# Performance work log

Hardware: AMD Instinct MI355X
Metric: run time of the kernel (lower is better)

## Reference

```python
import jax, jax.numpy as jnp
import numpy as np

T, D, H, E, K = 8192, 1024, 4096, 8, 2


def setup_inputs() -> dict:
    key = jax.random.key(0)
    ks = jax.random.split(key, 6)
    s_in = 1.0 / np.sqrt(D)
    s_hid = 1.0 / np.sqrt(H)
    return {
        "hidden_states": jax.random.normal(ks[0], (T, D), dtype=jnp.float32),
        "router_w": jax.random.normal(ks[1], (D, E), dtype=jnp.float32) * s_in,
        "expert_w1": jax.random.normal(ks[2], (E, D, H), dtype=jnp.float32) * s_in,
        "expert_w2": jax.random.normal(ks[3], (E, H, D), dtype=jnp.float32) * s_hid,
        "shared_w1": jax.random.normal(ks[4], (D, H), dtype=jnp.float32) * s_in,
        "shared_w2": jax.random.normal(ks[5], (H, D), dtype=jnp.float32) * s_hid,
    }


def reference(hidden_states, router_w, expert_w1, expert_w2, shared_w1, shared_w2):
    x = hidden_states  # [T, D]
    # --- router: softmax over experts, keep top-k, renormalize ---
    probs = jax.nn.softmax(x @ router_w, axis=-1)            # [T, E]
    top_v, top_i = jax.lax.top_k(probs, K)                   # [T, K]
    top_v = top_v / jnp.sum(top_v, axis=-1, keepdims=True)
    # dense combine weights [T, E]; zero for non-selected experts
    comb = jnp.zeros((x.shape[0], E), x.dtype).at[
        jnp.arange(x.shape[0])[:, None], top_i].set(top_v)
    # --- routed experts (dense reference for grouped GEMM) ---
    h = jax.nn.silu(jnp.einsum('td,edh->eth', x, expert_w1))  # [E, T, H]
    eo = jnp.einsum('eth,ehd->etd', h, expert_w2)             # [E, T, D]
    routed = jnp.einsum('te,etd->td', comb, eo)               # [T, D]
    # --- shared expert, always active ---
    shared = jax.nn.silu(x @ shared_w1) @ shared_w2           # [T, D]
    return routed + shared
```

## Files before the change

### kernel.cpp

```cpp
#include <hip/hip_runtime.h>
#include <hip/hip_bf16.h>
#include <stdint.h>

typedef unsigned short u16;
typedef __attribute__((ext_vector_type(8))) short bf16x8;
typedef __attribute__((ext_vector_type(4))) float f32x4;

constexpr int T_ = 8192;
constexpr int D_ = 1024;
constexpr int H_ = 4096;
constexpr int E_ = 8;
constexpr int NT_M  = 104;
constexpr int MAXR  = NT_M * 256;

__device__ __forceinline__ unsigned int f2bf_bits(float f) {
  unsigned int u = __float_as_uint(f);
  return (u + 0x7fffu + ((u >> 16) & 1u)) >> 16;
}
__device__ __forceinline__ float bf2f(u16 b) {
  return __uint_as_float(((unsigned int)b) << 16);
}

__device__ __forceinline__ void load_lds16(const void* g, void* s) {
  __builtin_amdgcn_global_load_lds(
      (const __attribute__((address_space(1))) unsigned int*)g,
      (__attribute__((address_space(3))) unsigned int*)s, 16, 0, 0);
}

__global__ __launch_bounds__(256) void router_kernel(
    const float* __restrict__ x, const float* __restrict__ rw,
    int* __restrict__ counts, int* __restrict__ tok2, float* __restrict__ wgt2) {
  __shared__ float rw_s[E_ * D_];
  __shared__ int c_s[E_];
  const int tid = threadIdx.x;
  if (tid < E_) c_s[tid] = 0;
  for (int f = tid; f < 2048; f += 256) {
    int d = f >> 1, p = f & 1;
    float4 v = *(const float4*)(rw + d * 8 + p * 4);
    rw_s[(p * 4 + 0) * D_ + d] = v.x;
    rw_s[(p * 4 + 1) * D_ + d] = v.y;
    rw_s[(p * 4 + 2) * D_ + d] = v.z;
    rw_s[(p * 4 + 3) * D_ + d] = v.w;
  }
  __syncthreads();
  const int wid = tid >> 6, lane = tid & 63;
  for (int ti = 0; ti < 16; ++ti) {
    const int t = blockIdx.x * 64 + wid * 16 + ti;
    const float* xr = x + (long)t * D_;
    float acc[E_] = {0.f, 0.f, 0.f, 0.f, 0.f, 0.f, 0.f, 0.f};
    for (int j = 0; j < 16; ++j) {
      const int d = lane + 64 * j;
      const float xv = xr[d];
#pragma unroll
      for (int e = 0; e < E_; ++e) acc[e] += xv * rw_s[e * D_ + d];
    }
#pragma unroll
    for (int off = 32; off >= 1; off >>= 1) {
#pragma unroll
      for (int e = 0; e < E_; ++e) acc[e] += __shfl_xor(acc[e], off, 64);
    }
    if (lane == 0) {
      int i0 = 0; float l0 = acc[0];
#pragma unroll
      for (int e = 1; e < E_; ++e) if (acc[e] > l0) { l0 = acc[e]; i0 = e; }
      int i1 = -1; float l1 = -3.4e38f;
#pragma unroll
      for (int e = 0; e < E_; ++e) if (e != i0 && acc[e] > l1) { l1 = acc[e]; i1 = e; }
      const float r = __expf(l1 - l0);
      const float inv = 1.f / (1.f + r);
      tok2[2 * t] = i0; tok2[2 * t + 1] = i1;
      wgt2[2 * t] = inv; wgt2[2 * t + 1] = r * inv;
      atomicAdd(&c_s[i0], 1); atomicAdd(&c_s[i1], 1);
    }
  }
  __syncthreads();
  if (tid < E_) atomicAdd(&counts[tid], c_s[tid]);
}

__global__ void scan_kernel(const int* __restrict__ counts, int* __restrict__ offs,
                            int* __restrict__ tile_expert, int* __restrict__ rowtok) {
  __shared__ int so[10];
  const int tid = threadIdx.x;
  if (tid == 0) {
    int o = 0;
    for (int e = 0; e < E_; ++e) { so[e] = o; o += ((counts[e] + 255) >> 8) << 8; }
    so[8] = o;
    o += T_;
    so[9] = o;
    for (int i = 0; i < 10; ++i) offs[i] = so[i];
  }
  __syncthreads();
  for (int i = tid; i < NT_M; i += 256) {
    const int row = i << 8;
    int e;
    if (row < so[8]) {
      e = 7;
      for (int k = 0; k < 7; ++k) if (row < so[k + 1]) { e = k; break; }
    } else if (row < so[9]) {
      e = 8;
    } else {
      e = -1;
    }
    tile_expert[i] = e;
  }
  for (int r = tid; r < MAXR; r += 256) rowtok[r] = 0;
}

__global__ __launch_bounds__(256) void assign_kernel(
    const int* __restrict__ tok2, const int* __restrict__ offs,
    int* __restrict__ cursors, int* __restrict__ rowtok, int* __restrict__ pos2) {
  __shared__ int lcnt[E_], lbase[E_];
  const int tid = threadIdx.x;
  if (tid < E_) lcnt[tid] = 0;
  __syncthreads();
  const int t = blockIdx.x * 256 + tid;
  const int e0 = tok2[2 * t], e1 = tok2[2 * t + 1];
  const int s0 = atomicAdd(&lcnt[e0], 1);
  const int s1 = atomicAdd(&lcnt[e1], 1);
  __syncthreads();
  if (tid < E_) lbase[tid] = offs[tid] + atomicAdd(&cursors[tid], lcnt[tid]);
  __syncthreads();
  const int p0 = lbase[e0] + s0, p1 = lbase[e1] + s1;
  rowtok[p0] = t; rowtok[p1] = t;
  pos2[2 * t] = p0; pos2[2 * t + 1] = p1;
  rowtok[offs[8] + t] = t;
}

__global__ __launch_bounds__(256) void cvt_x_kernel(const float* __restrict__ x,
                                                    u16* __restrict__ xb) {
  const long i = ((long)blockIdx.x * 256 + threadIdx.x) * 4;
  const float4 v = *(const float4*)(x + i);
  ushort4 o;
  o.x = (u16)f2bf_bits(v.x); o.y = (u16)f2bf_bits(v.y);
  o.z = (u16)f2bf_bits(v.z); o.w = (u16)f2bf_bits(v.w);
  *(ushort4*)(xb + i) = o;
}

__global__ __launch_bounds__(256) void transpose_cvt_kernel(
    const float* __restrict__ src8, const float* __restrict__ srcShared,
    u16* __restrict__ dst, int R, int C) {
  __shared__ float tile[64][65];
  const long stride = (long)R * C;
  const float* src = (blockIdx.z < 8) ? src8 + (long)blockIdx.z * stride : srcShared;
  u16* d = dst + (long)blockIdx.z * stride;
  const int tid = threadIdx.x;
  const int r0 = blockIdx.y * 64, c0 = blockIdx.x * 64;
  const int lr = tid >> 4, lc4 = tid & 15;
#pragma unroll
  for (int p = 0; p < 4; ++p) {
    const float4 v = *(const float4*)(src + (long)(r0 + lr + 16 * p) * C + c0 + lc4 * 4);
    tile[lr + 16 * p][lc4 * 4 + 0] = v.x;
    tile[lr + 16 * p][lc4 * 4 + 1] = v.y;
    tile[lr + 16 * p][lc4 * 4 + 2] = v.z;
    tile[lr + 16 * p][lc4 * 4 + 3] = v.w;
  }
  __syncthreads();
#pragma unroll
  for (int p = 0; p < 4; ++p) {
    const int rr = lr + 16 * p;
    ushort4 o;
    o.x = (u16)f2bf_bits(tile[lc4 * 4 + 0][rr]);
    o.y = (u16)f2bf_bits(tile[lc4 * 4 + 1][rr]);
    o.z = (u16)f2bf_bits(tile[lc4 * 4 + 2][rr]);
    o.w = (u16)f2bf_bits(tile[lc4 * 4 + 3][rr]);
    *(ushort4*)(d + (long)(c0 + rr) * R + r0 + lc4 * 4) = o;
  }
}

template <bool G1, int CHM>
__global__ __launch_bounds__(256, 2) void moe_gemm(
    const u16* __restrict__ A, const u16* __restrict__ Bt, u16* __restrict__ C,
    const int* __restrict__ rowtok, const int* __restrict__ tile_expert) {
  constexpr int K = G1 ? 1024 : 4096;
  constexpr int N = G1 ? 4096 : 1024;
  constexpr int NTn = N / 128;
  __shared__ u16 As[2 * 8192];
  __shared__ u16 Bs[2 * 4096];

  const int tid = threadIdx.x;
  int mt, nt;
  {
    const int bid = blockIdx.x;
    const int cb = CHM * NTn;
    const int chunk = bid / cb;
    const int mt0 = chunk * CHM;
    const int m = min(CHM, NT_M - mt0);
    const int rem = bid - chunk * cb;
    mt = mt0 + rem % m;
    nt = rem / m;
  }
  const int e = tile_expert[mt];
  if (e < 0) return;

  const int ric   = ((tid >> 6) << 4) | (tid & 15);
  const int sc    = ((tid >> 4) & 3) << 3;

  const u16* pa[4];
#pragma unroll
  for (int c = 0; c < 4; ++c) {
    const int grow = mt * 256 + c * 64 + ric;
    const long arow = G1 ? (long)rowtok[grow] : (long)grow;
    pa[c] = A + arow * K + sc;
  }
  const u16* pb[2];
#pragma unroll
  for (int c = 0; c < 2; ++c)
    pb[c] = Bt + (long)e * N * K + (long)(nt * 128 + c * 64 + ric) * K + sc;

  const int lane = tid & 63;
  const int wid = tid >> 6;
  const int wmh = wid >> 1;
  const int wnh = wid & 1;
  const int wm = wmh * 128, wn = wnh * 64;
  const int lr = lane & 15;
  const int quad = lane >> 4;
  const int lane8 = lane * 8;

  f32x4 acc[8][4] = {};

#pragma unroll
  for (int c = 0; c < 4; ++c) load_lds16(pa[c], As + c * 2048 + tid * 8);
#pragma unroll
  for (int c = 0; c < 2; ++c) load_lds16(pb[c], Bs + c * 2048 + tid * 8);

#pragma unroll 1
  for (int k0 = 0; k0 < K; k0 += 64) {
    __syncthreads();
    if (k0 + 32 < K) {
#pragma unroll
      for (int c = 0; c < 4; ++c)
        load_lds16(pa[c] + k0 + 32, As + 8192 + c * 2048 + tid * 8);
#pragma unroll
      for (int c = 0; c < 2; ++c)
        load_lds16(pb[c] + k0 + 32, Bs + 4096 + c * 2048 + tid * 8);
    }
    {
      bf16x8 af[8], bfv[4];
#pragma unroll
      for (int j = 0; j < 4; ++j)
        bfv[j] = *(const bf16x8*)(Bs + wnh * 2048 + j * 512 + lane8);
#pragma unroll
      for (int i = 0; i < 8; ++i)
        af[i] = *(const bf16x8*)(As + wmh * 4096 + i * 512 + lane8);
#pragma unroll
      for (int i = 0; i < 8; ++i)
#pragma unroll
        for (int j = 0; j < 4; ++j)
          acc[i][j] = __builtin_amdgcn_mfma_f32_16x16x32_bf16(af[i], bfv[j], acc[i][j], 0, 0, 0);
    }
    __syncthreads();
    if (k0 + 64 < K) {
#pragma unroll
      for (int c = 0; c < 4; ++c)
        load_lds16(pa[c] + k0 + 64, As + c * 2048 + tid * 8);
#pragma unroll
      for (int c = 0; c < 2; ++c)
        load_lds16(pb[c] + k0 + 64, Bs + c * 2048 + tid * 8);
    }
    {
      bf16x8 af[8], bfv[4];
#pragma unroll
      for (int j = 0; j < 4; ++j)
        bfv[j] = *(const bf16x8*)(Bs + 4096 + wnh * 2048 + j * 512 + lane8);
#pragma unroll
      for (int i = 0; i < 8; ++i)
        af[i] = *(const bf16x8*)(As + 8192 + wmh * 4096 + i * 512 + lane8);
#pragma unroll
      for (int i = 0; i < 8; ++i)
#pragma unroll
        for (int j = 0; j < 4; ++j)
          acc[i][j] = __builtin_amdgcn_mfma_f32_16x16x32_bf16(af[i], bfv[j], acc[i][j], 0, 0, 0);
    }
  }

  const int rbase = mt * 256 + wm + quad * 4;
#pragma unroll
  for (int i = 0; i < 8; ++i) {
#pragma unroll
    for (int j = 0; j < 4; ++j) {
#pragma unroll
      for (int r = 0; r < 4; ++r) {
        float v = acc[i][j][r];
        if constexpr (G1) v = v / (1.f + __expf(-v));
        unsigned int u = f2bf_bits(v);
        unsigned int other = (unsigned int)__shfl_xor((int)u, 1, 64);
        if (!(lane & 1)) {
          const unsigned int w = (u & 0xffffu) | (other << 16);
          const long row = rbase + i * 16 + r;
          const int col = nt * 128 + wn + j * 16 + lr;
          *(unsigned int*)(C + row * N + col) = w;
        }
      }
    }
  }
}

__global__ __launch_bounds__(256) void combine_kernel(
    const u16* __restrict__ eo, const int* __restrict__ pos2,
    const float* __restrict__ wgt2, const int* __restrict__ offs,
    float* __restrict__ out) {
  const int t = blockIdx.x, tid = threadIdx.x;
  const int p0 = pos2[2 * t], p1 = pos2[2 * t + 1];
  const float w0 = wgt2[2 * t], w1 = wgt2[2 * t + 1];
  const int ps = offs[8] + t;
  const long c = (long)tid * 4;
  const ushort4 a = *(const ushort4*)(eo + (long)p0 * D_ + c);
  const ushort4 b = *(const ushort4*)(eo + (long)p1 * D_ + c);
  const ushort4 s = *(const ushort4*)(eo + (long)ps * D_ + c);
  float4 o;
  o.x = w0 * bf2f(a.x) + w1 * bf2f(b.x) + bf2f(s.x);
  o.y = w0 * bf2f(a.y) + w1 * bf2f(b.y) + bf2f(s.y);
  o.z = w0 * bf2f(a.z) + w1 * bf2f(b.z) + bf2f(s.z);
  o.w = w0 * bf2f(a.w) + w1 * bf2f(b.w) + bf2f(s.w);
  *(float4*)(out + (long)t * D_ + c) = o;
}

extern "C" void kernel_launch(void* const* d_in, const int* in_sizes, int n_in,
                              void* d_out, int out_size, void* d_ws, size_t ws_size,
                              hipStream_t stream) {
  const float* x   = (const float*)d_in[0];
  const float* rw  = (const float*)d_in[1];
  const float* w1  = (const float*)d_in[2];
  const float* w2  = (const float*)d_in[3];
  const float* sw1 = (const float*)d_in[4];
  const float* sw2 = (const float*)d_in[5];
  float* out = (float*)d_out;

  char* ws = (char*)d_ws;
  int*   counts      = (int*)(ws + 0);
  int*   cursors     = (int*)(ws + 64);
  int*   offs        = (int*)(ws + 128);
  int*   tile_expert = (int*)(ws + 512);
  int*   tok2        = (int*)(ws + 4096);
  float* wgt2        = (float*)(ws + 4096 + 65536);
  int*   pos2        = (int*)(ws + 4096 + 131072);
  int*   rowtok      = (int*)(ws + 4096 + 196608);

  size_t off = 1u << 20;
  u16* xb  = (u16*)(ws + off); off += (size_t)T_ * D_ * 2;
  u16* w1t = (u16*)(ws + off); off += (size_t)9 * H_ * D_ * 2;
  u16* w2t = (u16*)(ws + off); off += (size_t)9 * D_ * H_ * 2;
  u16* h   = (u16*)(ws + off); off += (size_t)MAXR * H_ * 2;
  u16* eo  = (u16*)(ws + off); off += (size_t)MAXR * D_ * 2;

  hipMemsetAsync(ws, 0, 256, stream);
  router_kernel<<<128, 256, 0, stream>>>(x, rw, counts, tok2, wgt2);
  scan_kernel<<<1, 256, 0, stream>>>(counts, offs, tile_expert, rowtok);
  assign_kernel<<<32, 256, 0, stream>>>(tok2, offs, cursors, rowtok, pos2);
  cvt_x_kernel<<<T_ * D_ / 1024, 256, 0, stream>>>(x, xb);
  transpose_cvt_kernel<<<dim3(H_ / 64, D_ / 64, 9), 256, 0, stream>>>(w1, sw1, w1t, D_, H_);
  transpose_cvt_kernel<<<dim3(D_ / 64, H_ / 64, 9), 256, 0, stream>>>(w2, sw2, w2t, H_, D_);
  moe_gemm<true, 16><<<NT_M * (H_ / 128), 256, 0, stream>>>(xb, w1t, h, rowtok, tile_expert);
  moe_gemm<false, 16><<<NT_M * (D_ / 128), 256, 0, stream>>>(h, w2t, eo, rowtok, tile_expert);
  combine_kernel<<<T_, 256, 0, stream>>>(eo, pos2, wgt2, offs, out);
}
```

Baseline: 1.239 ms.

## Shrink MoE GEMM M-tile to 128 rows with 128-row expert padding

Halves the GEMM M-tile from 256 to 128 rows and pads each expert's row segment to 128 instead of 256. This cuts wasted padding rows and shrinks LDS use and accumulator registers, so launch bounds now allow four blocks per CU. The grouped-swizzle chunk sizes also change, to 24 for the first GEMM and 64 for the second. The trade-off is lower arithmetic intensity per tile: each B tile is reused across fewer rows, so more global and LDS traffic per flop.

```diff
diff --git a/kernel.cpp b/kernel.cpp
--- a/kernel.cpp
+++ b/kernel.cpp
@@ -10,8 +10,8 @@
 constexpr int D_ = 1024;
 constexpr int H_ = 4096;
 constexpr int E_ = 8;
-constexpr int NT_M  = 104;
-constexpr int MAXR  = NT_M * 256;
+constexpr int MAXROWS = 25600;
+constexpr int NTILES  = 200;
 
 __device__ __forceinline__ unsigned int f2bf_bits(float f) {
   unsigned int u = __float_as_uint(f);
@@ -83,15 +83,15 @@
   const int tid = threadIdx.x;
   if (tid == 0) {
     int o = 0;
-    for (int e = 0; e < E_; ++e) { so[e] = o; o += ((counts[e] + 255) >> 8) << 8; }
+    for (int e = 0; e < E_; ++e) { so[e] = o; o += ((counts[e] + 127) >> 7) << 7; }
     so[8] = o;
     o += T_;
     so[9] = o;
     for (int i = 0; i < 10; ++i) offs[i] = so[i];
   }
   __syncthreads();
-  for (int i = tid; i < NT_M; i += 256) {
-    const int row = i << 8;
+  for (int i = tid; i < NTILES; i += 256) {
+    const int row = i << 7;
     int e;
     if (row < so[8]) {
       e = 7;
@@ -103,7 +103,7 @@
     }
     tile_expert[i] = e;
   }
-  for (int r = tid; r < MAXR; r += 256) rowtok[r] = 0;
+  for (int r = tid; r < MAXROWS; r += 256) rowtok[r] = 0;
 }
 
 __global__ __launch_bounds__(256) void assign_kernel(
@@ -168,13 +168,13 @@
 }
 
 template <bool G1, int CHM>
-__global__ __launch_bounds__(256, 2) void moe_gemm(
+__global__ __launch_bounds__(256, 4) void moe_gemm(
     const u16* __restrict__ A, const u16* __restrict__ Bt, u16* __restrict__ C,
     const int* __restrict__ rowtok, const int* __restrict__ tile_expert) {
   constexpr int K = G1 ? 1024 : 4096;
   constexpr int N = G1 ? 4096 : 1024;
   constexpr int NTn = N / 128;
-  __shared__ u16 As[2 * 8192];
+  __shared__ u16 As[2 * 4096];
   __shared__ u16 Bs[2 * 4096];
 
   const int tid = threadIdx.x;
@@ -184,7 +184,7 @@
     const int cb = CHM * NTn;
     const int chunk = bid / cb;
     const int mt0 = chunk * CHM;
-    const int m = min(CHM, NT_M - mt0);
+    const int m = min(CHM, NTILES - mt0);
     const int rem = bid - chunk * cb;
     mt = mt0 + rem % m;
     nt = rem / m;
@@ -192,90 +192,87 @@
   const int e = tile_expert[mt];
   if (e < 0) return;
 
-  const int ric   = ((tid >> 6) << 4) | (tid & 15);
-  const int sc    = ((tid >> 4) & 3) << 3;
-
-  const u16* pa[4];
-#pragma unroll
-  for (int c = 0; c < 4; ++c) {
-    const int grow = mt * 256 + c * 64 + ric;
-    const long arow = G1 ? (long)rowtok[grow] : (long)grow;
-    pa[c] = A + arow * K + sc;
-  }
-  const u16* pb[2];
-#pragma unroll
-  for (int c = 0; c < 2; ++c)
-    pb[c] = Bt + (long)e * N * K + (long)(nt * 128 + c * 64 + ric) * K + sc;
+  const int ric = ((tid >> 6) << 4) | (tid & 15);
+  const int sc  = ((tid >> 4) & 3) << 3;
+
+  const u16* pa0;
+  const u16* pa1;
+  {
+    const int g0 = mt * 128 + ric;
+    const int g1 = g0 + 64;
+    const long r0 = G1 ? (long)rowtok[g0] : (long)g0;
+    const long r1 = G1 ? (long)rowtok[g1] : (long)g1;
+    pa0 = A + r0 * K + sc;
+    pa1 = A + r1 * K + sc;
+  }
+  const u16* pb0 = Bt + (long)e * N * K + (long)(nt * 128 + ric) * K + sc;
+  const u16* pb1 = pb0 + (long)64 * K;
 
   const int lane = tid & 63;
   const int wid = tid >> 6;
   const int wmh = wid >> 1;
   const int wnh = wid & 1;
-  const int wm = wmh * 128, wn = wnh * 64;
+  const int lane8 = lane * 8;
   const int lr = lane & 15;
   const int quad = lane >> 4;
-  const int lane8 = lane * 8;
-
-  f32x4 acc[8][4] = {};
-
-#pragma unroll
-  for (int c = 0; c < 4; ++c) load_lds16(pa[c], As + c * 2048 + tid * 8);
-#pragma unroll
-  for (int c = 0; c < 2; ++c) load_lds16(pb[c], Bs + c * 2048 + tid * 8);
+
+  f32x4 acc[4][4] = {};
+
+  load_lds16(pa0, As + tid * 8);
+  load_lds16(pa1, As + 2048 + tid * 8);
+  load_lds16(pb0, Bs + tid * 8);
+  load_lds16(pb1, Bs + 2048 + tid * 8);
 
 #pragma unroll 1
   for (int k0 = 0; k0 < K; k0 += 64) {
     __syncthreads();
     if (k0 + 32 < K) {
-#pragma unroll
-      for (int c = 0; c < 4; ++c)
-        load_lds16(pa[c] + k0 + 32, As + 8192 + c * 2048 + tid * 8);
-#pragma unroll
-      for (int c = 0; c < 2; ++c)
-        load_lds16(pb[c] + k0 + 32, Bs + 4096 + c * 2048 + tid * 8);
+      load_lds16(pa0 + k0 + 32, As + 4096 + tid * 8);
+      load_lds16(pa1 + k0 + 32, As + 4096 + 2048 + tid * 8);
+      load_lds16(pb0 + k0 + 32, Bs + 4096 + tid * 8);
+      load_lds16(pb1 + k0 + 32, Bs + 4096 + 2048 + tid * 8);
     }
     {
-      bf16x8 af[8], bfv[4];
+      bf16x8 af[4], bfv[4];
 #pragma unroll
       for (int j = 0; j < 4; ++j)
         bfv[j] = *(const bf16x8*)(Bs + wnh * 2048 + j * 512 + lane8);
 #pragma unroll
-      for (int i = 0; i < 8; ++i)
-        af[i] = *(const bf16x8*)(As + wmh * 4096 + i * 512 + lane8);
-#pragma unroll
-      for (int i = 0; i < 8; ++i)
+      for (int i = 0; i < 4; ++i)
+        af[i] = *(const bf16x8*)(As + wmh * 2048 + i * 512 + lane8);
+#pragma unroll
+      for (int i = 0; i < 4; ++i)
 #pragma unroll
         for (int j = 0; j < 4; ++j)
           acc[i][j] = __builtin_amdgcn_mfma_f32_16x16x32_bf16(af[i], bfv[j], acc[i][j], 0, 0, 0);
     }
     __syncthreads();
     if (k0 + 64 < K) {
-#pragma unroll
-      for (int c = 0; c < 4; ++c)
-        load_lds16(pa[c] + k0 + 64, As + c * 2048 + tid * 8);
-#pragma unroll
-      for (int c = 0; c < 2; ++c)
-        load_lds16(pb[c] + k0 + 64, Bs + c * 2048 + tid * 8);
+      load_lds16(pa0 + k0 + 64, As + tid * 8);
+      load_lds16(pa1 + k0 + 64, As + 2048 + tid * 8);
+      load_lds16(pb0 + k0 + 64, Bs + tid * 8);
+      load_lds16(pb1 + k0 + 64, Bs + 2048 + tid * 8);
     }
     {
-      bf16x8 af[8], bfv[4];
+      bf16x8 af[4], bfv[4];
 #pragma unroll
       for (int j = 0; j < 4; ++j)
         bfv[j] = *(const bf16x8*)(Bs + 4096 + wnh * 2048 + j * 512 + lane8);
 #pragma unroll
-      for (int i = 0; i < 8; ++i)
-        af[i] = *(const bf16x8*)(As + 8192 + wmh * 4096 + i * 512 + lane8);
-#pragma unroll
-      for (int i = 0; i < 8; ++i)
+      for (int i = 0; i < 4; ++i)
+        af[i] = *(const bf16x8*)(As + 4096 + wmh * 2048 + i * 512 + lane8);
+#pragma unroll
+      for (int i = 0; i < 4; ++i)
 #pragma unroll
         for (int j = 0; j < 4; ++j)
           acc[i][j] = __builtin_amdgcn_mfma_f32_16x16x32_bf16(af[i], bfv[j], acc[i][j], 0, 0, 0);
     }
   }
 
-  const int rbase = mt * 256 + wm + quad * 4;
-#pragma unroll
-  for (int i = 0; i < 8; ++i) {
+  const int rbase = mt * 128 + wmh * 64 + quad * 4;
+  const int cbase = nt * 128 + wnh * 64 + lr;
+#pragma unroll
+  for (int i = 0; i < 4; ++i) {
 #pragma unroll
     for (int j = 0; j < 4; ++j) {
 #pragma unroll
@@ -287,7 +284,7 @@
         if (!(lane & 1)) {
           const unsigned int w = (u & 0xffffu) | (other << 16);
           const long row = rbase + i * 16 + r;
-          const int col = nt * 128 + wn + j * 16 + lr;
+          const int col = cbase + j * 16;
           *(unsigned int*)(C + row * N + col) = w;
         }
       }
@@ -340,8 +337,8 @@
   u16* xb  = (u16*)(ws + off); off += (size_t)T_ * D_ * 2;
   u16* w1t = (u16*)(ws + off); off += (size_t)9 * H_ * D_ * 2;
   u16* w2t = (u16*)(ws + off); off += (size_t)9 * D_ * H_ * 2;
-  u16* h   = (u16*)(ws + off); off += (size_t)MAXR * H_ * 2;
-  u16* eo  = (u16*)(ws + off); off += (size_t)MAXR * D_ * 2;
+  u16* h   = (u16*)(ws + off); off += (size_t)MAXROWS * H_ * 2;
+  u16* eo  = (u16*)(ws + off); off += (size_t)MAXROWS * D_ * 2;
 
   hipMemsetAsync(ws, 0, 256, stream);
   router_kernel<<<128, 256, 0, stream>>>(x, rw, counts, tok2, wgt2);
@@ -350,7 +347,7 @@
   cvt_x_kernel<<<T_ * D_ / 1024, 256, 0, stream>>>(x, xb);
   transpose_cvt_kernel<<<dim3(H_ / 64, D_ / 64, 9), 256, 0, stream>>>(w1, sw1, w1t, D_, H_);
   transpose_cvt_kernel<<<dim3(D_ / 64, H_ / 64, 9), 256, 0, stream>>>(w2, sw2, w2t, H_, D_);
-  moe_gemm<true, 16><<<NT_M * (H_ / 128), 256, 0, stream>>>(xb, w1t, h, rowtok, tile_expert);
-  moe_gemm<false, 16><<<NT_M * (D_ / 128), 256, 0, stream>>>(h, w2t, eo, rowtok, tile_expert);
+  moe_gemm<true, 24><<<NTILES * (H_ / 128), 256, 0, stream>>>(xb, w1t, h, rowtok, tile_expert);
+  moe_gemm<false, 64><<<NTILES * (D_ / 128), 256, 0, stream>>>(h, w2t, eo, rowtok, tile_expert);
   combine_kernel<<<T_, 256, 0, stream>>>(eo, pos2, wgt2, offs, out);
 }
```

Measured after the change: 1.235 ms. About the same (-0.3%).
